# Kernel tuning notes

Measured on AMD Instinct MI355X. Metric: run time of the kernel, lower is better.

## Reference

```python
import jax, jax.numpy as jnp
import numpy as np

NEG_SLOPE = 0.2  # PyG GATConv default negative_slope
H1, H2, H3 = 4, 4, 1
CH = 64  # hidden_dim (per-head out channels)
N_NODES = 50000
N_EDGES = 800000
IN_DIM = 128
N_CLASSES = 10


def _gat_layer(x, src, dst, n, W, a_src, a_dst, b, heads, ch):
    # x: [N, Fin], W: [Fin, heads*ch], a_src/a_dst: [heads, ch], b: [heads*ch]
    h = (x @ W).reshape(-1, heads, ch)              # [N, H, C]
    e_src = jnp.sum(h * a_src, axis=-1)             # [N, H]
    e_dst = jnp.sum(h * a_dst, axis=-1)             # [N, H]
    e = jax.nn.leaky_relu(e_src[src] + e_dst[dst], NEG_SLOPE)  # [E, H]
    # segment softmax over incoming edges of each dst node
    m = jax.ops.segment_max(e, dst, num_segments=n)            # [N, H]
    p = jnp.exp(e - m[dst])                                    # [E, H]
    s = jax.ops.segment_sum(p, dst, num_segments=n)            # [N, H]
    alpha = p / (s[dst] + 1e-16)                               # [E, H]
    out = jax.ops.segment_sum(alpha[:, :, None] * h[src], dst, num_segments=n)  # [N, H, C]
    return out.reshape(-1, heads * ch) + b


def setup_inputs() -> dict:
    key = jax.random.key(0)
    ks = jax.random.split(key, 16)

    def glorot(k, shape, fan_in):
        return jax.random.normal(k, shape, dtype=jnp.float32) * (1.0 / np.sqrt(fan_in))

    x = jax.random.normal(ks[0], (N_NODES, IN_DIM), dtype=jnp.float32)
    edge_index = jax.random.randint(ks[1], (2, N_EDGES), 0, N_NODES, dtype=jnp.int32)

    d1 = H1 * CH  # 256
    d2 = H2 * CH  # 256
    d3 = H3 * CH  # 64
    return {
        "x": x,
        "edge_index": edge_index,
        "W1": glorot(ks[2], (IN_DIM, d1), IN_DIM),
        "a1_src": glorot(ks[3], (H1, CH), CH),
        "a1_dst": glorot(ks[4], (H1, CH), CH),
        "b1": jnp.zeros((d1,), jnp.float32),
        "W2": glorot(ks[5], (d1, d2), d1),
        "a2_src": glorot(ks[6], (H2, CH), CH),
        "a2_dst": glorot(ks[7], (H2, CH), CH),
        "b2": jnp.zeros((d2,), jnp.float32),
        "W3": glorot(ks[8], (d2, d3), d2),
        "a3_src": glorot(ks[9], (H3, CH), CH),
        "a3_dst": glorot(ks[10], (H3, CH), CH),
        "b3": jnp.zeros((d3,), jnp.float32),
        "fc_W": glorot(ks[11], (CH, N_CLASSES), CH),
        "fc_b": jnp.zeros((N_CLASSES,), jnp.float32),
    }


def reference(x, edge_index, W1, a1_src, a1_dst, b1, W2, a2_src, a2_dst, b2,
              W3, a3_src, a3_dst, b3, fc_W, fc_b):
    n = x.shape[0]
    # PyG GATConv adds self-loops by default
    loops = jnp.arange(n, dtype=edge_index.dtype)
    src = jnp.concatenate([edge_index[0], loops])
    dst = jnp.concatenate([edge_index[1], loops])

    h = jax.nn.relu(_gat_layer(x, src, dst, n, W1, a1_src, a1_dst, b1, H1, CH))
    # dropout(p=0.3) is identity in eval mode
    h = jax.nn.relu(_gat_layer(h, src, dst, n, W2, a2_src, a2_dst, b2, H2, CH))
    h = jax.nn.relu(_gat_layer(h, src, dst, n, W3, a3_src, a3_dst, b3, H3, CH))
    return h @ fc_W + fc_b  # [N, num_classes]
```

## Files before the change

### kernel.cpp

```cpp
#include <hip/hip_runtime.h>

#define NN 50000
#define NE 800000
#define E2 (NE + NN)
#define IN_DIM 128
#define SCAN_B 196

typedef unsigned short u16;
typedef unsigned int u32;
typedef __attribute__((ext_vector_type(8))) short short8;
typedef __attribute__((ext_vector_type(4))) float f32x4;

__device__ inline u16 f2bf(float x) {
    u32 u = __float_as_uint(x);
    u32 r = (u + 0x7fff + ((u >> 16) & 1)) >> 16;
    return (u16)r;
}
__device__ inline float bf2f(u16 h) { return __uint_as_float(((u32)h) << 16); }

__global__ __launch_bounds__(256) void fill_i32(int* __restrict__ p, int v, int n) {
    int i = blockIdx.x * 256 + threadIdx.x;
    if (i < n) p[i] = v;
}

__global__ __launch_bounds__(256) void hist_dst(const int* __restrict__ ei, int* __restrict__ deg) {
    int e = blockIdx.x * 256 + threadIdx.x;
    if (e < NE) atomicAdd(&deg[ei[NE + e]], 1);
}

__global__ __launch_bounds__(256) void block_sums(const int* __restrict__ deg, int* __restrict__ bsum) {
    int b = blockIdx.x;
    int i = b * 256 + threadIdx.x;
    int v = (i < NN) ? deg[i] : 0;
#pragma unroll
    for (int off = 32; off; off >>= 1) v += __shfl_down(v, off);
    __shared__ int ws[4];
    if ((threadIdx.x & 63) == 0) ws[threadIdx.x >> 6] = v;
    __syncthreads();
    if (threadIdx.x == 0) bsum[b] = ws[0] + ws[1] + ws[2] + ws[3];
}

__global__ __launch_bounds__(256) void scan_bsums(const int* __restrict__ bsum, int* __restrict__ boff) {
    __shared__ int s[256];
    int t = threadIdx.x;
    int v = (t < SCAN_B) ? bsum[t] : 0;
    s[t] = v;
    __syncthreads();
    for (int off = 1; off < 256; off <<= 1) {
        int u = (t >= off) ? s[t - off] : 0;
        __syncthreads();
        s[t] += u;
        __syncthreads();
    }
    if (t < SCAN_B) boff[t] = s[t] - v;
}

__global__ __launch_bounds__(256) void scan_final(const int* __restrict__ deg,
                                                  const int* __restrict__ boff,
                                                  int* __restrict__ rowptr,
                                                  int* __restrict__ cursor) {
    int b = blockIdx.x;
    int t = threadIdx.x;
    int i = b * 256 + t;
    int v = (i < NN) ? deg[i] : 0;
    __shared__ int s[256];
    s[t] = v;
    __syncthreads();
    for (int off = 1; off < 256; off <<= 1) {
        int u = (t >= off) ? s[t - off] : 0;
        __syncthreads();
        s[t] += u;
        __syncthreads();
    }
    int excl = s[t] - v + boff[b];
    if (i < NN) { rowptr[i] = excl; cursor[i] = excl; }
    if (i == NN - 1) rowptr[NN] = excl + v;
}

__global__ __launch_bounds__(256) void scatter_csr(const int* __restrict__ ei,
                                                   int* __restrict__ cursor,
                                                   int* __restrict__ csr_src) {
    int e = blockIdx.x * 256 + threadIdx.x;
    if (e >= E2) return;
    int s, d;
    if (e < NE) { s = ei[e]; d = ei[NE + e]; } else { s = d = e - NE; }
    int pos = atomicAdd(&cursor[d], 1);
    csr_src[pos] = s;
}

__global__ __launch_bounds__(256) void xconv(const float* __restrict__ X,
                                             u16* __restrict__ Xh, u16* __restrict__ Xl,
                                             int total4) {
    int i = blockIdx.x * 256 + threadIdx.x;
    if (i >= total4) return;
    float4 v = reinterpret_cast<const float4*>(X)[i];
    ushort4 h, l;
    h.x = f2bf(v.x); l.x = f2bf(v.x - bf2f(h.x));
    h.y = f2bf(v.y); l.y = f2bf(v.y - bf2f(h.y));
    h.z = f2bf(v.z); l.z = f2bf(v.z - bf2f(h.z));
    h.w = f2bf(v.w); l.w = f2bf(v.w - bf2f(h.w));
    reinterpret_cast<ushort4*>(Xh)[i] = h;
    reinterpret_cast<ushort4*>(Xl)[i] = l;
}

__global__ __launch_bounds__(256) void wconv(const float* __restrict__ W,
                                             u16* __restrict__ Wh, u16* __restrict__ Wl,
                                             int K, int N) {
    int idx = blockIdx.x * 256 + threadIdx.x;
    if (idx >= K * N) return;
    int k = idx / N, n = idx - k * N;
    float w = W[idx];
    u16 hi = f2bf(w);
    Wh[(size_t)n * K + k] = hi;
    Wl[(size_t)n * K + k] = f2bf(w - bf2f(hi));
}

template<int BN, int KK, bool FES>
__global__ __launch_bounds__(256) void gemm_mfma(const u16* __restrict__ Ah,
                                                 const u16* __restrict__ Al,
                                                 const u16* __restrict__ Wh,
                                                 const u16* __restrict__ Wl,
                                                 float* __restrict__ C,
                                                 int M, int N,
                                                 const float* __restrict__ as_,
                                                 const float* __restrict__ ad_,
                                                 float* __restrict__ es,
                                                 float* __restrict__ ed) {
    const int BM = 128, BK = 32, LDT = BK + 8;
    __shared__ u16 Ahs[2][BM][LDT], Als[2][BM][LDT];
    const int FRN = BN / 32;
    int tid = threadIdx.x;
    int lane = tid & 63, wid = tid >> 6;
    int wm = wid >> 1, wn = wid & 1;
    int row0 = blockIdx.x * BM, col0 = blockIdx.y * BN;
    int l15 = lane & 15, lg = lane >> 4;

    int c0 = tid * 2;
    int r_a = c0 >> 2, sub_a0 = (c0 & 3) * 8, sub_a1 = ((c0 + 1) & 3) * 8;
    int gr_a = row0 + r_a;

    uint4 avh[2], avl[2];
    auto loadA = [&](int ko) {
        if (gr_a < M) {
            avh[0] = *reinterpret_cast<const uint4*>(Ah + (size_t)gr_a * KK + ko + sub_a0);
            avl[0] = *reinterpret_cast<const uint4*>(Al + (size_t)gr_a * KK + ko + sub_a0);
            avh[1] = *reinterpret_cast<const uint4*>(Ah + (size_t)gr_a * KK + ko + sub_a1);
            avl[1] = *reinterpret_cast<const uint4*>(Al + (size_t)gr_a * KK + ko + sub_a1);
        } else {
            avh[0] = avh[1] = avl[0] = avl[1] = make_uint4(0, 0, 0, 0);
        }
    };
    auto writeA = [&](int p) {
        *reinterpret_cast<uint4*>(&Ahs[p][r_a][sub_a0]) = avh[0];
        *reinterpret_cast<uint4*>(&Als[p][r_a][sub_a0]) = avl[0];
        *reinterpret_cast<uint4*>(&Ahs[p][r_a][sub_a1]) = avh[1];
        *reinterpret_cast<uint4*>(&Als[p][r_a][sub_a1]) = avl[1];
    };

    f32x4 acc[4][FRN];
#pragma unroll
    for (int i = 0; i < 4; ++i)
#pragma unroll
        for (int j = 0; j < FRN; ++j) acc[i][j] = (f32x4){0.f, 0.f, 0.f, 0.f};

    loadA(0);
    writeA(0);
    loadA(BK);
    __syncthreads();

    for (int ko = 0; ko < KK; ko += BK) {
        int p = (ko >> 5) & 1;
        if (ko + BK < KK) {
            writeA(p ^ 1);
            if (ko + 2 * BK < KK) loadA(ko + 2 * BK);
        }
        short8 bh[FRN], bl[FRN];
#pragma unroll
        for (int j = 0; j < FRN; ++j) {
            int gc = col0 + wn * (BN / 2) + j * 16 + l15;
            bh[j] = *reinterpret_cast<const short8*>(Wh + (size_t)gc * KK + ko + lg * 8);
            bl[j] = *reinterpret_cast<const short8*>(Wl + (size_t)gc * KK + ko + lg * 8);
        }
        short8 ah[4], al[4];
#pragma unroll
        for (int i = 0; i < 4; ++i) {
            int r = wm * 64 + i * 16 + l15;
            ah[i] = *reinterpret_cast<const short8*>(&Ahs[p][r][lg * 8]);
            al[i] = *reinterpret_cast<const short8*>(&Als[p][r][lg * 8]);
        }
#pragma unroll
        for (int i = 0; i < 4; ++i)
#pragma unroll
            for (int j = 0; j < FRN; ++j) {
                acc[i][j] = __builtin_amdgcn_mfma_f32_16x16x32_bf16(ah[i], bh[j], acc[i][j], 0, 0, 0);
                acc[i][j] = __builtin_amdgcn_mfma_f32_16x16x32_bf16(ah[i], bl[j], acc[i][j], 0, 0, 0);
                acc[i][j] = __builtin_amdgcn_mfma_f32_16x16x32_bf16(al[i], bh[j], acc[i][j], 0, 0, 0);
            }
        __syncthreads();
    }
#pragma unroll
    for (int i = 0; i < 4; ++i)
#pragma unroll
        for (int rr = 0; rr < 4; ++rr) {
            int gr = row0 + wm * 64 + i * 16 + lg * 4 + rr;
            if (gr < M) {
#pragma unroll
                for (int j = 0; j < FRN; ++j)
                    C[(size_t)gr * N + col0 + wn * (BN / 2) + j * 16 + l15] = acc[i][j][rr];
            }
        }
    if (FES) {
        if constexpr (BN == 128) {
            int head = (col0 + wn * (BN / 2)) >> 6;
            float asv[FRN], adv[FRN];
#pragma unroll
            for (int j = 0; j < FRN; ++j) {
                asv[j] = as_[head * 64 + j * 16 + l15];
                adv[j] = ad_[head * 64 + j * 16 + l15];
            }
#pragma unroll
            for (int i = 0; i < 4; ++i)
#pragma unroll
                for (int rr = 0; rr < 4; ++rr) {
                    float vs = 0.f, vd = 0.f;
#pragma unroll
                    for (int j = 0; j < FRN; ++j) {
                        vs += acc[i][j][rr] * asv[j];
                        vd += acc[i][j][rr] * adv[j];
                    }
#pragma unroll
                    for (int off = 1; off < 16; off <<= 1) {
                        vs += __shfl_xor(vs, off);
                        vd += __shfl_xor(vd, off);
                    }
                    int gr = row0 + wm * 64 + i * 16 + lg * 4 + rr;
                    if (l15 == 0 && gr < M) {
                        es[gr * 4 + head] = vs;
                        ed[gr * 4 + head] = vd;
                    }
                }
        } else {
            __shared__ float esp[2][BM], edp[2][BM];
            float asv[FRN], adv[FRN];
#pragma unroll
            for (int j = 0; j < FRN; ++j) {
                asv[j] = as_[wn * (BN / 2) + j * 16 + l15];
                adv[j] = ad_[wn * (BN / 2) + j * 16 + l15];
            }
#pragma unroll
            for (int i = 0; i < 4; ++i)
#pragma unroll
                for (int rr = 0; rr < 4; ++rr) {
                    float vs = 0.f, vd = 0.f;
#pragma unroll
                    for (int j = 0; j < FRN; ++j) {
                        vs += acc[i][j][rr] * asv[j];
                        vd += acc[i][j][rr] * adv[j];
                    }
#pragma unroll
                    for (int off = 1; off < 16; off <<= 1) {
                        vs += __shfl_xor(vs, off);
                        vd += __shfl_xor(vd, off);
                    }
                    int rl = wm * 64 + i * 16 + lg * 4 + rr;
                    if (l15 == 0) { esp[wn][rl] = vs; edp[wn][rl] = vd; }
                }
            __syncthreads();
            if (tid < BM) {
                int gr = row0 + tid;
                if (gr < M) {
                    es[gr] = esp[0][tid] + esp[1][tid];
                    ed[gr] = edp[0][tid] + edp[1][tid];
                }
            }
        }
    }
}

template<int D, int H, bool FC>
__global__ __launch_bounds__(256) void agg_fused(const int* __restrict__ rowptr,
                                                 const int* __restrict__ csr_src,
                                                 const float* __restrict__ es,
                                                 const float* __restrict__ ed,
                                                 const float* __restrict__ h,
                                                 const float* __restrict__ b,
                                                 u16* __restrict__ Oh,
                                                 u16* __restrict__ Ol,
                                                 const float* __restrict__ fcW,
                                                 const float* __restrict__ fcb,
                                                 float* __restrict__ out) {
    const int TPN = D / 4;
    const int NPB = 256 / TPN;
    const int logH = (H == 4) ? 2 : 0;
    int tid = threadIdx.x;
    int n = blockIdx.x * NPB + tid / TPN;
    if (n >= NN) return;
    int gl = tid % TPN;
    int start = rowptr[n], end = rowptr[n + 1];

    int headA = gl & (H - 1);
    const int JP = TPN >> logH;
    float edvA = ed[n * H + headA];
    float m = -1e30f;
    for (int i = start + (gl >> logH); i < end; i += JP) {
        int src = csr_src[i];
        float v = es[src * H + headA] + edvA;
        v = v > 0.f ? v : 0.2f * v;
        m = fmaxf(m, v);
    }
#pragma unroll
    for (int off = H; off < TPN; off <<= 1)
        m = fmaxf(m, __shfl_xor(m, off));

    int f0 = gl * 4;
    int hb = f0 >> 6;
    float mB;
    if (D == 256) mB = __shfl(m, hb);
    else          mB = m;
    float edv = ed[n * H + hb];
    float sump = 0.f;
    float4 acc = make_float4(0.f, 0.f, 0.f, 0.f);
    int i = start;
    for (; i + 8 <= end; i += 8) {
        int s0 = csr_src[i + 0], s1 = csr_src[i + 1], s2 = csr_src[i + 2], s3 = csr_src[i + 3];
        int s4 = csr_src[i + 4], s5 = csr_src[i + 5], s6 = csr_src[i + 6], s7 = csr_src[i + 7];
        float v0 = es[s0 * H + hb] + edv, v1 = es[s1 * H + hb] + edv;
        float v2 = es[s2 * H + hb] + edv, v3 = es[s3 * H + hb] + edv;
        float v4 = es[s4 * H + hb] + edv, v5 = es[s5 * H + hb] + edv;
        float v6 = es[s6 * H + hb] + edv, v7 = es[s7 * H + hb] + edv;
        v0 = v0 > 0.f ? v0 : 0.2f * v0; v1 = v1 > 0.f ? v1 : 0.2f * v1;
        v2 = v2 > 0.f ? v2 : 0.2f * v2; v3 = v3 > 0.f ? v3 : 0.2f * v3;
        v4 = v4 > 0.f ? v4 : 0.2f * v4; v5 = v5 > 0.f ? v5 : 0.2f * v5;
        v6 = v6 > 0.f ? v6 : 0.2f * v6; v7 = v7 > 0.f ? v7 : 0.2f * v7;
        float p0 = __expf(v0 - mB), p1 = __expf(v1 - mB);
        float p2 = __expf(v2 - mB), p3 = __expf(v3 - mB);
        float p4 = __expf(v4 - mB), p5 = __expf(v5 - mB);
        float p6 = __expf(v6 - mB), p7 = __expf(v7 - mB);
        float4 h0 = *reinterpret_cast<const float4*>(h + (size_t)s0 * D + f0);
        float4 h1 = *reinterpret_cast<const float4*>(h + (size_t)s1 * D + f0);
        float4 h2 = *reinterpret_cast<const float4*>(h + (size_t)s2 * D + f0);
        float4 h3 = *reinterpret_cast<const float4*>(h + (size_t)s3 * D + f0);
        float4 h4 = *reinterpret_cast<const float4*>(h + (size_t)s4 * D + f0);
        float4 h5 = *reinterpret_cast<const float4*>(h + (size_t)s5 * D + f0);
        float4 h6 = *reinterpret_cast<const float4*>(h + (size_t)s6 * D + f0);
        float4 h7 = *reinterpret_cast<const float4*>(h + (size_t)s7 * D + f0);
        acc.x += p0 * h0.x + p1 * h1.x + p2 * h2.x + p3 * h3.x
               + p4 * h4.x + p5 * h5.x + p6 * h6.x + p7 * h7.x;
        acc.y += p0 * h0.y + p1 * h1.y + p2 * h2.y + p3 * h3.y
               + p4 * h4.y + p5 * h5.y + p6 * h6.y + p7 * h7.y;
        acc.z += p0 * h0.z + p1 * h1.z + p2 * h2.z + p3 * h3.z
               + p4 * h4.z + p5 * h5.z + p6 * h6.z + p7 * h7.z;
        acc.w += p0 * h0.w + p1 * h1.w + p2 * h2.w + p3 * h3.w
               + p4 * h4.w + p5 * h5.w + p6 * h6.w + p7 * h7.w;
        sump += p0 + p1 + p2 + p3 + p4 + p5 + p6 + p7;
    }
    for (; i < end; ++i) {
        int s0 = csr_src[i];
        float v = es[s0 * H + hb] + edv;
        v = v > 0.f ? v : 0.2f * v;
        float p = __expf(v - mB);
        float4 h0 = *reinterpret_cast<const float4*>(h + (size_t)s0 * D + f0);
        acc.x += p * h0.x; acc.y += p * h0.y; acc.z += p * h0.z; acc.w += p * h0.w;
        sump += p;
    }
    float inv = 1.f / (sump + 1e-16f);
    float4 bb = *reinterpret_cast<const float4*>(b + f0);
    float4 o;
    o.x = acc.x * inv + bb.x; o.y = acc.y * inv + bb.y;
    o.z = acc.z * inv + bb.z; o.w = acc.w * inv + bb.w;
    o.x = o.x > 0.f ? o.x : 0.f; o.y = o.y > 0.f ? o.y : 0.f;
    o.z = o.z > 0.f ? o.z : 0.f; o.w = o.w > 0.f ? o.w : 0.f;
    if (!FC) {
        ushort4 hv, lv;
        hv.x = f2bf(o.x); lv.x = f2bf(o.x - bf2f(hv.x));
        hv.y = f2bf(o.y); lv.y = f2bf(o.y - bf2f(hv.y));
        hv.z = f2bf(o.z); lv.z = f2bf(o.z - bf2f(hv.z));
        hv.w = f2bf(o.w); lv.w = f2bf(o.w - bf2f(hv.w));
        *reinterpret_cast<ushort4*>(Oh + (size_t)n * D + f0) = hv;
        *reinterpret_cast<ushort4*>(Ol + (size_t)n * D + f0) = lv;
    } else {
        float pj[10];
#pragma unroll
        for (int j = 0; j < 10; ++j)
            pj[j] = o.x * fcW[(f0 + 0) * 10 + j] + o.y * fcW[(f0 + 1) * 10 + j]
                  + o.z * fcW[(f0 + 2) * 10 + j] + o.w * fcW[(f0 + 3) * 10 + j];
#pragma unroll
        for (int off = 1; off < 16; off <<= 1)
#pragma unroll
            for (int j = 0; j < 10; ++j)
                pj[j] += __shfl_xor(pj[j], off);
        if (gl < 10) {
            float r = 0.f;
#pragma unroll
            for (int j = 0; j < 10; ++j) if (gl == j) r = pj[j];
            out[n * 10 + gl] = r + fcb[gl];
        }
    }
}

extern "C" void kernel_launch(void* const* d_in, const int* in_sizes, int n_in,
                              void* d_out, int out_size, void* d_ws, size_t ws_size,
                              hipStream_t stream) {
    const float* x   = (const float*)d_in[0];
    const int*   ei  = (const int*)d_in[1];
    const float* W1  = (const float*)d_in[2];
    const float* a1s = (const float*)d_in[3];
    const float* a1d = (const float*)d_in[4];
    const float* b1  = (const float*)d_in[5];
    const float* W2  = (const float*)d_in[6];
    const float* a2s = (const float*)d_in[7];
    const float* a2d = (const float*)d_in[8];
    const float* b2  = (const float*)d_in[9];
    const float* W3  = (const float*)d_in[10];
    const float* a3s = (const float*)d_in[11];
    const float* a3d = (const float*)d_in[12];
    const float* b3  = (const float*)d_in[13];
    const float* fcW = (const float*)d_in[14];
    const float* fcb = (const float*)d_in[15];
    float* out = (float*)d_out;

    char* wp = (char*)d_ws;
    float* h   = (float*)wp;  wp += (size_t)NN * 256 * 4;
    u16* Ph    = (u16*)wp;    wp += (size_t)NN * 256 * 2;
    u16* Pl    = (u16*)wp;    wp += (size_t)NN * 256 * 2;
    u16* Xh    = (u16*)wp;    wp += (size_t)NN * 128 * 2;
    u16* Xl    = (u16*)wp;    wp += (size_t)NN * 128 * 2;
    float* ES  = (float*)wp;  wp += (size_t)NN * 4 * 4;
    float* ED  = (float*)wp;  wp += (size_t)NN * 4 * 4;
    u16* Wth   = (u16*)wp;    wp += 256 * 256 * 2;
    u16* Wtl   = (u16*)wp;    wp += 256 * 256 * 2;
    int* rowptr = (int*)wp;   wp += (NN + 1) * 4;
    int* csrsrc = (int*)wp;   wp += (size_t)E2 * 4;
    int* deg    = (int*)wp;   wp += NN * 4;
    int* bsum   = (int*)wp;   wp += 256 * 4;
    int* boff   = (int*)wp;   wp += 256 * 4;
    int* cursor = (int*)((char*)d_ws + (size_t)NN * 256 * 4);

    fill_i32<<<(NN + 255) / 256, 256, 0, stream>>>(deg, 1, NN);
    hist_dst<<<(NE + 255) / 256, 256, 0, stream>>>(ei, deg);
    block_sums<<<SCAN_B, 256, 0, stream>>>(deg, bsum);
    scan_bsums<<<1, 256, 0, stream>>>(bsum, boff);
    scan_final<<<SCAN_B, 256, 0, stream>>>(deg, boff, rowptr, cursor);
    scatter_csr<<<(E2 + 255) / 256, 256, 0, stream>>>(ei, cursor, csrsrc);

    xconv<<<(NN * IN_DIM / 4 + 255) / 256, 256, 0, stream>>>(x, Xh, Xl, NN * IN_DIM / 4);

    const int MT = (NN + 127) / 128;

    wconv<<<(IN_DIM * 256 + 255) / 256, 256, 0, stream>>>(W1, Wth, Wtl, IN_DIM, 256);
    gemm_mfma<128, 128, true><<<dim3(MT, 2), 256, 0, stream>>>(Xh, Xl, Wth, Wtl, h, NN, 256,
                                                               a1s, a1d, ES, ED);
    agg_fused<256, 4, false><<<(NN + 3) / 4, 256, 0, stream>>>(rowptr, csrsrc, ES, ED, h, b1,
                                                               Ph, Pl, nullptr, nullptr, nullptr);

    wconv<<<(256 * 256 + 255) / 256, 256, 0, stream>>>(W2, Wth, Wtl, 256, 256);
    gemm_mfma<128, 256, true><<<dim3(MT, 2), 256, 0, stream>>>(Ph, Pl, Wth, Wtl, h, NN, 256,
                                                               a2s, a2d, ES, ED);
    agg_fused<256, 4, false><<<(NN + 3) / 4, 256, 0, stream>>>(rowptr, csrsrc, ES, ED, h, b2,
                                                               Ph, Pl, nullptr, nullptr, nullptr);

    wconv<<<(256 * 64 + 255) / 256, 256, 0, stream>>>(W3, Wth, Wtl, 256, 64);
    gemm_mfma<64, 256, true><<<dim3(MT, 1), 256, 0, stream>>>(Ph, Pl, Wth, Wtl, h, NN, 64,
                                                              a3s, a3d, ES, ED);
    agg_fused<64, 1, true><<<(NN + 15) / 16, 256, 0, stream>>>(rowptr, csrsrc, ES, ED, h, b3,
                                                               nullptr, nullptr, fcW, fcb, out);
}
```

Baseline: 526.7 us.

## Load GEMM A fragments directly from global memory, dropping LDS staging and barriers

The split-bf16 MFMA GEMM no longer stages A tiles through double-buffered shared memory. Each wave now loads its A fragments straight from global memory into registers, as it already did for B, with out-of-range rows clamped to the last row. This removes the LDS writes and reads and the per-iteration __syncthreads. The cost is that A rows are fetched by both column-half waves instead of being shared, and the explicit prefetch pipeline is lost, so more global or L2 traffic and more exposed latency are possible.

Result: slower. 546.1 us (+3.7%).

```diff
diff --git a/kernel.cpp b/kernel.cpp
--- a/kernel.cpp
+++ b/kernel.cpp
@@ -126,8 +126,7 @@
                                                  const float* __restrict__ ad_,
                                                  float* __restrict__ es,
                                                  float* __restrict__ ed) {
-    const int BM = 128, BK = 32, LDT = BK + 8;
-    __shared__ u16 Ahs[2][BM][LDT], Als[2][BM][LDT];
+    const int BM = 128;
     const int FRN = BN / 32;
     int tid = threadIdx.x;
     int lane = tid & 63, wid = tid >> 6;
@@ -135,58 +134,42 @@
     int row0 = blockIdx.x * BM, col0 = blockIdx.y * BN;
     int l15 = lane & 15, lg = lane >> 4;
 
-    int c0 = tid * 2;
-    int r_a = c0 >> 2, sub_a0 = (c0 & 3) * 8, sub_a1 = ((c0 + 1) & 3) * 8;
-    int gr_a = row0 + r_a;
-
-    uint4 avh[2], avl[2];
-    auto loadA = [&](int ko) {
-        if (gr_a < M) {
-            avh[0] = *reinterpret_cast<const uint4*>(Ah + (size_t)gr_a * KK + ko + sub_a0);
-            avl[0] = *reinterpret_cast<const uint4*>(Al + (size_t)gr_a * KK + ko + sub_a0);
-            avh[1] = *reinterpret_cast<const uint4*>(Ah + (size_t)gr_a * KK + ko + sub_a1);
-            avl[1] = *reinterpret_cast<const uint4*>(Al + (size_t)gr_a * KK + ko + sub_a1);
-        } else {
-            avh[0] = avh[1] = avl[0] = avl[1] = make_uint4(0, 0, 0, 0);
+    const u16* aph[4];
+    const u16* apl[4];
+#pragma unroll
+    for (int i = 0; i < 4; ++i) {
+        int r = row0 + wm * 64 + i * 16 + l15;
+        if (r > M - 1) r = M - 1;
+        aph[i] = Ah + (size_t)r * KK + lg * 8;
+        apl[i] = Al + (size_t)r * KK + lg * 8;
+    }
+    const u16* bph[FRN];
+    const u16* bpl[FRN];
+#pragma unroll
+    for (int j = 0; j < FRN; ++j) {
+        int gc = col0 + wn * (BN / 2) + j * 16 + l15;
+        bph[j] = Wh + (size_t)gc * KK + lg * 8;
+        bpl[j] = Wl + (size_t)gc * KK + lg * 8;
+    }
+
+    f32x4 acc[4][FRN];
+#pragma unroll
+    for (int i = 0; i < 4; ++i)
+#pragma unroll
+        for (int j = 0; j < FRN; ++j) acc[i][j] = (f32x4){0.f, 0.f, 0.f, 0.f};
+
+#pragma unroll 2
+    for (int ko = 0; ko < KK; ko += 32) {
+        short8 ah[4], al[4], bh[FRN], bl[FRN];
+#pragma unroll
+        for (int i = 0; i < 4; ++i) {
+            ah[i] = *reinterpret_cast<const short8*>(aph[i] + ko);
+            al[i] = *reinterpret_cast<const short8*>(apl[i] + ko);
         }
-    };
-    auto writeA = [&](int p) {
-        *reinterpret_cast<uint4*>(&Ahs[p][r_a][sub_a0]) = avh[0];
-        *reinterpret_cast<uint4*>(&Als[p][r_a][sub_a0]) = avl[0];
-        *reinterpret_cast<uint4*>(&Ahs[p][r_a][sub_a1]) = avh[1];
-        *reinterpret_cast<uint4*>(&Als[p][r_a][sub_a1]) = avl[1];
-    };
-
-    f32x4 acc[4][FRN];
-#pragma unroll
-    for (int i = 0; i < 4; ++i)
-#pragma unroll
-        for (int j = 0; j < FRN; ++j) acc[i][j] = (f32x4){0.f, 0.f, 0.f, 0.f};
-
-    loadA(0);
-    writeA(0);
-    loadA(BK);
-    __syncthreads();
-
-    for (int ko = 0; ko < KK; ko += BK) {
-        int p = (ko >> 5) & 1;
-        if (ko + BK < KK) {
-            writeA(p ^ 1);
-            if (ko + 2 * BK < KK) loadA(ko + 2 * BK);
-        }
-        short8 bh[FRN], bl[FRN];
 #pragma unroll
         for (int j = 0; j < FRN; ++j) {
-            int gc = col0 + wn * (BN / 2) + j * 16 + l15;
-            bh[j] = *reinterpret_cast<const short8*>(Wh + (size_t)gc * KK + ko + lg * 8);
-            bl[j] = *reinterpret_cast<const short8*>(Wl + (size_t)gc * KK + ko + lg * 8);
-        }
-        short8 ah[4], al[4];
-#pragma unroll
-        for (int i = 0; i < 4; ++i) {
-            int r = wm * 64 + i * 16 + l15;
-            ah[i] = *reinterpret_cast<const short8*>(&Ahs[p][r][lg * 8]);
-            al[i] = *reinterpret_cast<const short8*>(&Als[p][r][lg * 8]);
+            bh[j] = *reinterpret_cast<const short8*>(bph[j] + ko);
+            bl[j] = *reinterpret_cast<const short8*>(bpl[j] + ko);
         }
 #pragma unroll
         for (int i = 0; i < 4; ++i)
@@ -196,7 +179,6 @@
                 acc[i][j] = __builtin_amdgcn_mfma_f32_16x16x32_bf16(ah[i], bl[j], acc[i][j], 0, 0, 0);
                 acc[i][j] = __builtin_amdgcn_mfma_f32_16x16x32_bf16(al[i], bh[j], acc[i][j], 0, 0, 0);
             }
-        __syncthreads();
     }
 #pragma unroll
     for (int i = 0; i < 4; ++i)
```
